# Kernel tuning notes

Hardware: AMD Instinct MI355X
Metric: run time of the kernel (lower is better)

Reference implementation:

```python
import jax, jax.numpy as jnp
import numpy as np

B, H, W, C = 16, 64, 64, 512
NH, HD = 16, 32
WH = WW = 8
SHIFT = 4
N = WH * WW
NWIN = (H // WH) * (W // WW)
EPS = 1e-6


def _rel_coords_table():
    rh = np.arange(-(WH - 1), WH, dtype=np.float32)
    rw = np.arange(-(WW - 1), WW, dtype=np.float32)
    t = np.expand_dims(np.transpose(np.stack(np.meshgrid(rh, rw)), (1, 2, 0)), 0)
    t[:, :, :, 0] /= WH - 1
    t[:, :, :, 1] /= WW - 1
    t *= 8
    t = np.sign(t) * np.log2(np.abs(t) + 1.0) / np.log2(8)
    return jnp.asarray(t, jnp.float32)  # (1, 2*WW-1, 2*WH-1, 2)


def _rel_pos_index():
    gx, gy = np.meshgrid(np.arange(WH), np.arange(WW))
    coords = np.stack([gy, gx]).reshape(2, -1)
    rel = (coords[:, :, None] - coords[:, None, :]).transpose(1, 2, 0)
    rel[:, :, 0] += WH - 1
    rel[:, :, 1] += WW - 1
    rel[:, :, 0] *= 2 * WW - 1
    return jnp.asarray(rel.sum(-1).reshape(-1), jnp.int32)  # (N*N,)


def _attn_mask():
    img = np.zeros((H, W), np.float32)
    cnt = 0
    for hs in (slice(0, -WH), slice(-WH, -SHIFT), slice(-SHIFT, None)):
        for ws in (slice(0, -WW), slice(-WW, -SHIFT), slice(-SHIFT, None)):
            img[hs, ws] = cnt
            cnt += 1
    mw = img.reshape(H // WH, WH, W // WW, WW).transpose(0, 2, 1, 3).reshape(-1, N)
    am = mw[:, None, :] - mw[:, :, None]
    return jnp.asarray(np.where(am == 0, 0.0, -100.0), jnp.float32)  # (nW, N, N)


REL_TABLE = _rel_coords_table()
REL_IDX = _rel_pos_index()
ATTN_MASK = _attn_mask()


def _ln(x, g, b):
    m = jnp.mean(x, -1, keepdims=True)
    v = jnp.var(x, -1, keepdims=True)
    return (x - m) * jax.lax.rsqrt(v + EPS) * g + b


def _forward(x, q_w, q_b, k_w, v_w, v_b, proj_w, proj_b, tau,
             cpb_w1, cpb_b1, cpb_w2, cpb_b2,
             norm1_g, norm1_b, norm2_g, norm2_b,
             mlp_w1, mlp_b1, mlp_w2, mlp_b2):
    shortcut = x
    xs = x.reshape(B, H, W, C)
    xs = jnp.roll(xs, shift=(-SHIFT, -SHIFT), axis=(1, 2))  # cyclic shift
    # window partition -> (B*nW, N, C)
    xw = xs.reshape(B, H // WH, WH, W // WW, WW, C).transpose(0, 1, 3, 2, 4, 5).reshape(-1, N, C)
    Bw = B * NWIN
    q = (xw @ q_w + q_b).reshape(Bw, N, NH, HD).transpose(0, 2, 1, 3)
    k = (xw @ k_w).reshape(Bw, N, NH, HD).transpose(0, 2, 1, 3)
    v = (xw @ v_w + v_b).reshape(Bw, N, NH, HD).transpose(0, 2, 1, 3)
    # cosine attention
    qn = jnp.linalg.norm(q, axis=-1)[..., :, None]
    kn = jnp.linalg.norm(k, axis=-1)[..., None, :]
    denom = jnp.maximum(qn * kn, 1e-6)
    attn = jnp.einsum('bhnd,bhmd->bhnm', q, k) / denom
    logit_scale = jnp.maximum(tau + jnp.log(10.0), 0.01)  # (1, NH, 1, 1)
    attn = attn * logit_scale
    # continuous relative position bias MLP
    tbl = jax.nn.relu(REL_TABLE @ cpb_w1 + cpb_b1) @ cpb_w2 + cpb_b2
    tbl = tbl.reshape(-1, NH)
    bias = tbl[REL_IDX].reshape(N, N, NH).transpose(2, 0, 1)
    bias = 16.0 * jax.nn.sigmoid(bias)
    attn = attn + bias[None]
    # shifted-window mask
    attn = attn.reshape(B, NWIN, NH, N, N) + ATTN_MASK[None, :, None]
    attn = jax.nn.softmax(attn.reshape(Bw, NH, N, N), axis=-1)
    out = jnp.einsum('bhnm,bhmd->bhnd', attn, v).transpose(0, 2, 1, 3).reshape(Bw, N, C)
    out = out @ proj_w + proj_b
    # window reverse + reverse shift
    out = out.reshape(B, H // WH, W // WW, WH, WW, C).transpose(0, 1, 3, 2, 4, 5).reshape(B, H, W, C)
    out = jnp.roll(out, shift=(SHIFT, SHIFT), axis=(1, 2)).reshape(B, H * W, C)
    # Swin-V2 post-norm residuals
    x = shortcut + _ln(out, norm1_g, norm1_b)
    h = jax.nn.gelu(x @ mlp_w1 + mlp_b1) @ mlp_w2 + mlp_b2
    x = x + _ln(h, norm2_g, norm2_b)
    return x


def setup_inputs() -> dict:
    key = jax.random.key(0)
    ks = jax.random.split(key, 10)
    s = 0.02
    return {
        'x': jax.random.normal(ks[0], (B, H * W, C), jnp.float32),
        'q_w': jax.random.normal(ks[1], (C, C), jnp.float32) * s,
        'q_b': jnp.zeros((C,), jnp.float32),
        'k_w': jax.random.normal(ks[2], (C, C), jnp.float32) * s,
        'v_w': jax.random.normal(ks[3], (C, C), jnp.float32) * s,
        'v_b': jnp.zeros((C,), jnp.float32),
        'proj_w': jax.random.normal(ks[4], (C, C), jnp.float32) * s,
        'proj_b': jnp.zeros((C,), jnp.float32),
        'tau': jax.random.normal(ks[5], (1, NH, 1, 1), jnp.float32) * s,
        'cpb_w1': jax.random.normal(ks[6], (2, 512), jnp.float32) * s,
        'cpb_b1': jnp.zeros((512,), jnp.float32),
        'cpb_w2': jax.random.normal(ks[7], (512, NH), jnp.float32) * s,
        'cpb_b2': jnp.zeros((NH,), jnp.float32),
        'norm1_g': jnp.ones((C,), jnp.float32),
        'norm1_b': jnp.zeros((C,), jnp.float32),
        'norm2_g': jnp.ones((C,), jnp.float32),
        'norm2_b': jnp.zeros((C,), jnp.float32),
        'mlp_w1': jax.random.normal(ks[8], (C, 4 * C), jnp.float32) * s,
        'mlp_b1': jnp.zeros((4 * C,), jnp.float32),
        'mlp_w2': jax.random.normal(ks[9], (4 * C, C), jnp.float32) * s,
        'mlp_b2': jnp.zeros((C,), jnp.float32),
    }


def reference(x, q_w, q_b, k_w, v_w, v_b, proj_w, proj_b, tau,
              cpb_w1, cpb_b1, cpb_w2, cpb_b2,
              norm1_g, norm1_b, norm2_g, norm2_b,
              mlp_w1, mlp_b1, mlp_w2, mlp_b2):
    return _forward(x, q_w, q_b, k_w, v_w, v_b, proj_w, proj_b, tau,
                    cpb_w1, cpb_b1, cpb_w2, cpb_b2,
                    norm1_g, norm1_b, norm2_g, norm2_b,
                    mlp_w1, mlp_b1, mlp_w2, mlp_b2)
```

## Files before the change

### kernel.cpp

```cpp
#include <hip/hip_runtime.h>
#include <cstdint>
#include <cstddef>

typedef __bf16 bf16x8 __attribute__((ext_vector_type(8)));
typedef float  f32x4  __attribute__((ext_vector_type(4)));
typedef unsigned short u16x8 __attribute__((ext_vector_type(8)));

__device__ __forceinline__ float bf2f(unsigned short u) {
  union { unsigned int u; float f; } v; v.u = ((unsigned int)u) << 16; return v.f;
}
__device__ __forceinline__ unsigned short f2bf(float f) {
  union { float f; unsigned int u; } v; v.f = f;
  return (unsigned short)((v.u + 0x7fffu + ((v.u >> 16) & 1u)) >> 16);
}
__device__ __forceinline__ bf16x8 as_bf(u16x8 u) {
  union { u16x8 a; bf16x8 b; } v; v.a = u; return v.b;
}
__device__ __forceinline__ void g2lds16(const void* g, void* l) {
  __builtin_amdgcn_global_load_lds((__attribute__((address_space(1))) void*)g,
                                   (__attribute__((address_space(3))) void*)l,
                                   16, 0, 0);
}

template<int EPI>
__global__ __launch_bounds__(512, 2) void gemm256(
    const unsigned short* __restrict__ A, const unsigned short* __restrict__ BT,
    const float* __restrict__ bias, unsigned short* __restrict__ C,
    int M, int N, int K)
{
  __shared__ __align__(16) unsigned short lds[2][2][2][128 * 64];
  const int tid = threadIdx.x;
  const int wave = tid >> 6, lane = tid & 63;
  const int lm = lane & 15, quad = lane >> 4;
  const int wm2 = wave >> 2, wn4 = wave & 3;
  const int ex = (lm & 7) << 3;

  const int nbx = (int)gridDim.x;
  const int nwg = nbx * (int)gridDim.y;
  const int flat = (int)blockIdx.y * nbx + (int)blockIdx.x;
  const int cpx = nwg >> 3;
  const int wg = (flat & 7) * cpx + (flat >> 3);
  const int bm = wg / nbx, bn = wg % nbx;

  const int NT = K >> 6;

  const int sl8 = lane >> 3;
  const int scol = ((lane & 7) ^ sl8) << 3;
  const int r0 = wave * 8 + sl8;
  const unsigned short* Abase = A + (size_t)(bm * 256 + r0) * K + scol;
  const unsigned short* Bbase = BT + (size_t)(bn * 256 + (r0 >> 5) * 64 + (r0 & 31)) * K + scol;

  auto stageA = [&](int bf, int sh, int koff) {
    const unsigned short* s = Abase + (size_t)(sh * 64) * K + koff;
    g2lds16(s,                   &lds[bf][0][sh][wave * 512]);
    g2lds16(s + (size_t)128 * K, &lds[bf][0][sh][4096 + wave * 512]);
  };
  auto stageB = [&](int bf, int sh, int koff) {
    const unsigned short* s = Bbase + (size_t)(sh * 32) * K + koff;
    g2lds16(s,                   &lds[bf][1][sh][wave * 512]);
    g2lds16(s + (size_t)128 * K, &lds[bf][1][sh][4096 + wave * 512]);
  };

  f32x4 acc[8][4];
#pragma unroll
  for (int i = 0; i < 8; i++)
#pragma unroll
    for (int j = 0; j < 4; j++) acc[i][j] = {0.f, 0.f, 0.f, 0.f};
  bf16x8 a[4][2], b0[2][2], b1[2][2];

  stageA(0, 0, 0); stageB(0, 0, 0); stageB(0, 1, 0); stageA(0, 1, 0);
  {
    const int k1 = (NT > 1 ? 64 : 0);
    stageA(1, 0, k1); stageB(1, 0, k1);
  }
  asm volatile("s_waitcnt vmcnt(4)" ::: "memory");
  __builtin_amdgcn_s_barrier();

  for (int t = 0; t < NT; ++t) {
    const int b = t & 1;
    const int kn1 = (t + 1 < NT ? t + 1 : NT - 1) << 6;
    const int kn2 = (t + 2 < NT ? t + 2 : NT - 1) << 6;

#pragma unroll
    for (int mi = 0; mi < 4; mi++)
#pragma unroll
      for (int ks = 0; ks < 2; ks++)
        a[mi][ks] = *(const bf16x8*)&lds[b][0][0][(wm2 * 64 + mi * 16 + lm) * 64 + ((ks * 32 + quad * 8) ^ ex)];
#pragma unroll
    for (int ni = 0; ni < 2; ni++)
#pragma unroll
      for (int ks = 0; ks < 2; ks++)
        b0[ni][ks] = *(const bf16x8*)&lds[b][1][0][(wn4 * 32 + ni * 16 + lm) * 64 + ((ks * 32 + quad * 8) ^ ex)];
    stageB(b ^ 1, 1, kn1);
    __builtin_amdgcn_s_barrier();
    __builtin_amdgcn_s_setprio(1);
#pragma unroll
    for (int mi = 0; mi < 4; mi++)
#pragma unroll
      for (int ni = 0; ni < 2; ni++)
#pragma unroll
        for (int ks = 0; ks < 2; ks++)
          acc[mi][ni] = __builtin_amdgcn_mfma_f32_16x16x32_bf16(a[mi][ks], b0[ni][ks], acc[mi][ni], 0, 0, 0);
    __builtin_amdgcn_s_setprio(0);
    asm volatile("s_waitcnt vmcnt(8)" ::: "memory");
    __builtin_amdgcn_s_barrier();

#pragma unroll
    for (int ni = 0; ni < 2; ni++)
#pragma unroll
      for (int ks = 0; ks < 2; ks++)
        b1[ni][ks] = *(const bf16x8*)&lds[b][1][1][(wn4 * 32 + ni * 16 + lm) * 64 + ((ks * 32 + quad * 8) ^ ex)];
    stageA(b ^ 1, 1, kn1);
    __builtin_amdgcn_s_barrier();
    __builtin_amdgcn_s_setprio(1);
#pragma unroll
    for (int mi = 0; mi < 4; mi++)
#pragma unroll
      for (int ni = 0; ni < 2; ni++)
#pragma unroll
        for (int ks = 0; ks < 2; ks++)
          acc[mi][2 + ni] = __builtin_amdgcn_mfma_f32_16x16x32_bf16(a[mi][ks], b1[ni][ks], acc[mi][2 + ni], 0, 0, 0);
    __builtin_amdgcn_s_setprio(0);
    asm volatile("s_waitcnt vmcnt(8)" ::: "memory");
    __builtin_amdgcn_s_barrier();

#pragma unroll
    for (int mi = 0; mi < 4; mi++)
#pragma unroll
      for (int ks = 0; ks < 2; ks++)
        a[mi][ks] = *(const bf16x8*)&lds[b][0][1][(wm2 * 64 + mi * 16 + lm) * 64 + ((ks * 32 + quad * 8) ^ ex)];
    stageA(b, 0, kn2);
    __builtin_amdgcn_s_barrier();
    __builtin_amdgcn_s_setprio(1);
#pragma unroll
    for (int mi = 0; mi < 4; mi++)
#pragma unroll
      for (int ni = 0; ni < 2; ni++)
#pragma unroll
        for (int ks = 0; ks < 2; ks++)
          acc[4 + mi][ni] = __builtin_amdgcn_mfma_f32_16x16x32_bf16(a[mi][ks], b0[ni][ks], acc[4 + mi][ni], 0, 0, 0);
    __builtin_amdgcn_s_setprio(0);
    asm volatile("s_waitcnt vmcnt(8)" ::: "memory");
    __builtin_amdgcn_s_barrier();

    stageB(b, 0, kn2);
    __builtin_amdgcn_s_barrier();
    __builtin_amdgcn_s_setprio(1);
#pragma unroll
    for (int mi = 0; mi < 4; mi++)
#pragma unroll
      for (int ni = 0; ni < 2; ni++)
#pragma unroll
        for (int ks = 0; ks < 2; ks++)
          acc[4 + mi][2 + ni] = __builtin_amdgcn_mfma_f32_16x16x32_bf16(a[mi][ks], b1[ni][ks], acc[4 + mi][2 + ni], 0, 0, 0);
    __builtin_amdgcn_s_setprio(0);
    asm volatile("s_waitcnt vmcnt(8)" ::: "memory");
    __builtin_amdgcn_s_barrier();
  }

  float bv[4];
#pragma unroll
  for (int jn = 0; jn < 4; jn++)
    bv[jn] = bias ? bias[bn * 256 + wn4 * 64 + jn * 16 + lm] : 0.f;
  const int rb = bm * 256 + wm2 * 128 + quad * 4;
  const int cb = bn * 256 + wn4 * 64 + lm;
#pragma unroll
  for (int im = 0; im < 8; im++)
#pragma unroll
    for (int jn = 0; jn < 4; jn++)
#pragma unroll
      for (int r = 0; r < 4; r++) {
        float v = acc[im][jn][r] + bv[jn];
        if (EPI == 1) {
          float xx = v;
          float u = 1.5957691216057308f * (xx + 0.044715f * xx * xx * xx);
          v = xx / (1.f + __expf(-u));
        }
        C[(size_t)(rb + im * 16 + r) * N + cb + jn * 16] = f2bf(v);
      }
}

__global__ __launch_bounds__(256) void transpose_cast(
    const float* __restrict__ W, unsigned short* __restrict__ WT, int K, int N)
{
  __shared__ float t[32][33];
  int bx = blockIdx.x, by = blockIdx.y;
  int tx = threadIdx.x & 31, ty = threadIdx.x >> 5;
#pragma unroll
  for (int j = 0; j < 4; j++)
    t[ty + j * 8][tx] = W[(size_t)(by * 32 + ty + j * 8) * N + bx * 32 + tx];
  __syncthreads();
#pragma unroll
  for (int j = 0; j < 4; j++)
    WT[(size_t)(bx * 32 + ty + j * 8) * K + by * 32 + tx] = f2bf(t[tx][ty + j * 8]);
}

__global__ __launch_bounds__(256) void shift_part(
    const float* __restrict__ x, unsigned short* __restrict__ xw)
{
  int t = blockIdx.x * 256 + threadIdx.x;
  int row = t >> 7;
  int c = (t & 127) * 4;
  int b = row >> 12, rw_ = row & 4095;
  int wi = rw_ >> 6, p = rw_ & 63;
  int hh = (((wi >> 3) * 8 + (p >> 3)) + 4) & 63;
  int ww = (((wi & 7) * 8 + (p & 7)) + 4) & 63;
  const float4 v = *(const float4*)&x[(((size_t)b * 4096) + hh * 64 + ww) * 512 + c];
  ushort4 o;
  o.x = f2bf(v.x); o.y = f2bf(v.y); o.z = f2bf(v.z); o.w = f2bf(v.w);
  *(ushort4*)&xw[(size_t)row * 512 + c] = o;
}

__global__ __launch_bounds__(256) void qkv_bias_kernel(
    const float* __restrict__ qb, const float* __restrict__ vb, float* __restrict__ o)
{
  int t = blockIdx.x * 256 + threadIdx.x;
  float v = 0.f;
  if (t < 512) v = qb[t];
  else if (t >= 1024) v = vb[t - 1024];
  o[t] = v;
}

__device__ __forceinline__ float relsc(int v) {
  float a = fabsf((float)v) * (8.0f / 7.0f);
  float r = log2f(a + 1.f) * (1.f / 3.f);
  return v < 0 ? -r : r;
}
__global__ __launch_bounds__(512) void cpb_kernel(
    const float* __restrict__ w1, const float* __restrict__ b1,
    const float* __restrict__ w2, const float* __restrict__ b2, float* __restrict__ tblT)
{
  __shared__ float hid[512];
  int p = blockIdx.x;
  int i = p / 15, j = p % 15;
  float fr = relsc(i - 7);
  float fc = relsc(j - 7);
  int t = threadIdx.x;
  float hv = fc * w1[t] + fr * w1[512 + t] + b1[t];
  hid[t] = fmaxf(hv, 0.f);
  __syncthreads();
  if (t < 16) {
    float s = b2[t];
    for (int u = 0; u < 512; u++) s += hid[u] * w2[u * 16 + t];
    tblT[t * 225 + p] = 16.f / (1.f + __expf(-s));
  }
}

__global__ __launch_bounds__(256) void attn_mfma(
    const unsigned short* __restrict__ QKV, const float* __restrict__ tau,
    const float* __restrict__ tblT, unsigned short* __restrict__ Om)
{
  __shared__ __align__(16) unsigned short Qs[64 * 32];
  __shared__ __align__(16) unsigned short Ks[64 * 32];
  __shared__ __align__(16) unsigned short Vs[64 * 32];
  __shared__ __align__(16) unsigned short VT[32 * 72];
  __shared__ __align__(16) unsigned short Pb[64 * 72];
  __shared__ float tblh[2][228];
  __shared__ int scode[64];

  const int tid = threadIdx.x;
  const int wave = tid >> 6, lane = tid & 63;
  const int lm = lane & 15, quad = lane >> 4;
  const int w = blockIdx.x >> 1;
  const int hbase = (blockIdx.x & 1) * 8;
  const int wi = w & 63, wr = wi >> 3, wc = wi & 7;
  const size_t wbase = (size_t)w * 64 * 1536;
  const size_t obase = (size_t)w * 64 * 512;

  if (tid < 64) {
    int p = tid;
    int rp = wr * 8 + (p >> 3), cp = wc * 8 + (p & 7);
    scode[p] = (rp < 56 ? 0 : (rp < 60 ? 1 : 2)) * 3 + (cp < 56 ? 0 : (cp < 60 ? 1 : 2));
  }

  const int srow = wave * 16 + (lane >> 2);
  const int scol = (lane & 3) * 8;
  unsigned short* qdst = &Qs[wave * 16 * 32];
  unsigned short* kdst = &Ks[wave * 16 * 32];
  unsigned short* vdst = &Vs[wave * 16 * 32];
  const size_t gs0 = wbase + (size_t)srow * 1536 + scol;

  {
    const size_t g = gs0 + (size_t)hbase * 32;
    g2lds16(QKV + g, qdst);
    g2lds16(QKV + g + 512, kdst);
    g2lds16(QKV + g + 1024, vdst);
    for (int e = tid; e < 225; e += 256) tblh[0][e] = tblT[hbase * 225 + e];
  }

  for (int hh = 0; hh < 8; hh++) {
    const int h = hbase + hh, cur = hh & 1;
    __syncthreads();

    u16x8 au = *(const u16x8*)&Qs[(wave * 16 + lm) * 32 + quad * 8];
    float qss = 0.f;
#pragma unroll
    for (int j = 0; j < 8; j++) { float f = bf2f(au[j]); qss += f * f; }
    qss += __shfl_xor(qss, 16, 64);
    qss += __shfl_xor(qss, 32, 64);
    const float qnv = sqrtf(qss);

    u16x8 bu[4]; float knv[4];
#pragma unroll
    for (int ni = 0; ni < 4; ni++) {
      bu[ni] = *(const u16x8*)&Ks[(ni * 16 + lm) * 32 + quad * 8];
      float kss = 0.f;
#pragma unroll
      for (int j = 0; j < 8; j++) { float f = bf2f(bu[ni][j]); kss += f * f; }
      kss += __shfl_xor(kss, 16, 64);
      kss += __shfl_xor(kss, 32, 64);
      knv[ni] = sqrtf(kss);
    }

    bf16x8 af = as_bf(au);
    f32x4 accS[4];
#pragma unroll
    for (int ni = 0; ni < 4; ni++) {
      f32x4 z = {0.f, 0.f, 0.f, 0.f};
      accS[ni] = __builtin_amdgcn_mfma_f32_16x16x32_bf16(af, as_bf(bu[ni]), z, 0, 0, 0);
    }

    for (int e = tid; e < 2048; e += 256) {
      int d = e & 31, q = e >> 5;
      VT[d * 72 + q] = Vs[q * 32 + d];
    }

    const float scale = fmaxf(tau[h] + 2.302585092994046f, 0.01f);
#pragma unroll
    for (int r = 0; r < 4; r++) {
      int p = wave * 16 + quad * 4 + r;
      float qnp = __shfl(qnv, quad * 4 + r, 64);
      int cp = scode[p];
      float sv[4];
#pragma unroll
      for (int ni = 0; ni < 4; ni++) {
        int q = ni * 16 + lm;
        float denom = fmaxf(qnp * knv[ni], 1e-6f);
        int dr = (p >> 3) - (q >> 3) + 7, dc = (p & 7) - (q & 7) + 7;
        float bv = tblh[cur][dr * 15 + dc];
        float mask = (cp == scode[q]) ? 0.f : -100.f;
        sv[ni] = accS[ni][r] * scale * __builtin_amdgcn_rcpf(denom) + bv + mask;
      }
      float m = fmaxf(fmaxf(sv[0], sv[1]), fmaxf(sv[2], sv[3]));
#pragma unroll
      for (int off = 1; off < 16; off <<= 1) m = fmaxf(m, __shfl_xor(m, off, 64));
      float s = 0.f;
#pragma unroll
      for (int ni = 0; ni < 4; ni++) { sv[ni] = __expf(sv[ni] - m); s += sv[ni]; }
#pragma unroll
      for (int off = 1; off < 16; off <<= 1) s += __shfl_xor(s, off, 64);
      float inv = __builtin_amdgcn_rcpf(s);
#pragma unroll
      for (int ni = 0; ni < 4; ni++)
        Pb[p * 72 + ni * 16 + lm] = f2bf(sv[ni] * inv);
    }

    __syncthreads();

    if (hh < 7) {
      const size_t g = gs0 + (size_t)(h + 1) * 32;
      g2lds16(QKV + g, qdst);
      g2lds16(QKV + g + 512, kdst);
      g2lds16(QKV + g + 1024, vdst);
      for (int e = tid; e < 225; e += 256) tblh[cur ^ 1][e] = tblT[(h + 1) * 225 + e];
    }

    bf16x8 paf[2];
#pragma unroll
    for (int kc = 0; kc < 2; kc++)
      paf[kc] = *reinterpret_cast<const bf16x8*>(&Pb[(wave * 16 + lm) * 72 + kc * 32 + quad * 8]);
    f32x4 accO[2];
#pragma unroll
    for (int n2 = 0; n2 < 2; n2++) {
      f32x4 z = {0.f, 0.f, 0.f, 0.f};
#pragma unroll
      for (int kc = 0; kc < 2; kc++) {
        bf16x8 vb = *reinterpret_cast<const bf16x8*>(&VT[(n2 * 16 + lm) * 72 + kc * 32 + quad * 8]);
        z = __builtin_amdgcn_mfma_f32_16x16x32_bf16(paf[kc], vb, z, 0, 0, 0);
      }
      accO[n2] = z;
    }
#pragma unroll
    for (int n2 = 0; n2 < 2; n2++)
#pragma unroll
      for (int r = 0; r < 4; r++) {
        int p = wave * 16 + quad * 4 + r;
        Om[obase + (size_t)p * 512 + h * 32 + n2 * 16 + lm] = f2bf(accO[n2][r]);
      }
  }
}

__global__ __launch_bounds__(256) void ln1_kernel(
    const float* __restrict__ x, const unsigned short* __restrict__ proj,
    const float* __restrict__ g, const float* __restrict__ b,
    unsigned short* __restrict__ x1b)
{
  __shared__ float r1[4], r2[4], stats[2];
  int tkn = blockIdx.x;
  int bb = tkn >> 12, s = tkn & 4095;
  int h_ = s >> 6, w_ = s & 63;
  int r = (h_ + 60) & 63, cc = (w_ + 60) & 63;
  int wi = (r >> 3) * 8 + (cc >> 3);
  int p = (r & 7) * 8 + (cc & 7);
  size_t src = ((size_t)bb * 4096 + wi * 64 + p) * 512;
  int c = threadIdx.x * 2;
  unsigned int pv = *(const unsigned int*)&proj[src + c];
  float v0 = bf2f((unsigned short)(pv & 0xffff)), v1 = bf2f((unsigned short)(pv >> 16));
  float ls = v0 + v1, lq = v0 * v0 + v1 * v1;
  for (int off = 32; off > 0; off >>= 1) {
    ls += __shfl_down(ls, off, 64);
    lq += __shfl_down(lq, off, 64);
  }
  int wv = threadIdx.x >> 6, ln = threadIdx.x & 63;
  if (ln == 0) { r1[wv] = ls; r2[wv] = lq; }
  __syncthreads();
  if (threadIdx.x == 0) {
    float S1 = r1[0] + r1[1] + r1[2] + r1[3];
    float S2 = r2[0] + r2[1] + r2[2] + r2[3];
    float mean = S1 * (1.f / 512.f);
    float var = S2 * (1.f / 512.f) - mean * mean;
    stats[0] = mean; stats[1] = rsqrtf(var + 1e-6f);
  }
  __syncthreads();
  float mean = stats[0], rstd = stats[1];
  size_t o = (size_t)tkn * 512 + c;
  float2 xv = *(const float2*)&x[o];
  float y0 = (v0 - mean) * rstd * g[c] + b[c] + xv.x;
  float y1 = (v1 - mean) * rstd * g[c + 1] + b[c + 1] + xv.y;
  unsigned int ov = (unsigned int)f2bf(y0) | ((unsigned int)f2bf(y1) << 16);
  *(unsigned int*)&x1b[o] = ov;
}

__global__ __launch_bounds__(256) void ln2_kernel(
    const unsigned short* __restrict__ x1b, const unsigned short* __restrict__ h2,
    const float* __restrict__ g, const float* __restrict__ b,
    float* __restrict__ out)
{
  __shared__ float r1[4], r2[4], stats[2];
  int tkn = blockIdx.x;
  int c = threadIdx.x * 2;
  size_t o = (size_t)tkn * 512 + c;
  unsigned int hv = *(const unsigned int*)&h2[o];
  float v0 = bf2f((unsigned short)(hv & 0xffff)), v1 = bf2f((unsigned short)(hv >> 16));
  float ls = v0 + v1, lq = v0 * v0 + v1 * v1;
  for (int off = 32; off > 0; off >>= 1) {
    ls += __shfl_down(ls, off, 64);
    lq += __shfl_down(lq, off, 64);
  }
  int wv = threadIdx.x >> 6, ln = threadIdx.x & 63;
  if (ln == 0) { r1[wv] = ls; r2[wv] = lq; }
  __syncthreads();
  if (threadIdx.x == 0) {
    float S1 = r1[0] + r1[1] + r1[2] + r1[3];
    float S2 = r2[0] + r2[1] + r2[2] + r2[3];
    float mean = S1 * (1.f / 512.f);
    float var = S2 * (1.f / 512.f) - mean * mean;
    stats[0] = mean; stats[1] = rsqrtf(var + 1e-6f);
  }
  __syncthreads();
  float mean = stats[0], rstd = stats[1];
  unsigned int xv = *(const unsigned int*)&x1b[o];
  float x0 = bf2f((unsigned short)(xv & 0xffff)), x1 = bf2f((unsigned short)(xv >> 16));
  float2 ov;
  ov.x = x0 + (v0 - mean) * rstd * g[c] + b[c];
  ov.y = x1 + (v1 - mean) * rstd * g[c + 1] + b[c + 1];
  *(float2*)&out[o] = ov;
}

extern "C" void kernel_launch(void* const* d_in, const int* in_sizes, int n_in,
                              void* d_out, int out_size, void* d_ws, size_t ws_size,
                              hipStream_t stream) {
  const float* x      = (const float*)d_in[0];
  const float* q_w    = (const float*)d_in[1];
  const float* q_b    = (const float*)d_in[2];
  const float* k_w    = (const float*)d_in[3];
  const float* v_w    = (const float*)d_in[4];
  const float* v_b    = (const float*)d_in[5];
  const float* proj_w = (const float*)d_in[6];
  const float* proj_b = (const float*)d_in[7];
  const float* tau    = (const float*)d_in[8];
  const float* cpb_w1 = (const float*)d_in[9];
  const float* cpb_b1 = (const float*)d_in[10];
  const float* cpb_w2 = (const float*)d_in[11];
  const float* cpb_b2 = (const float*)d_in[12];
  const float* n1g    = (const float*)d_in[13];
  const float* n1b    = (const float*)d_in[14];
  const float* n2g    = (const float*)d_in[15];
  const float* n2b    = (const float*)d_in[16];
  const float* mlp_w1 = (const float*)d_in[17];
  const float* mlp_b1 = (const float*)d_in[18];
  const float* mlp_w2 = (const float*)d_in[19];
  const float* mlp_b2 = (const float*)d_in[20];
  float* out = (float*)d_out;
  char* ws = (char*)d_ws;

  const size_t MB = 1048576;
  unsigned short* xw    = (unsigned short*)(ws + 0 * MB);
  unsigned short* Obuf  = (unsigned short*)(ws + 0 * MB);
  unsigned short* hbuf  = (unsigned short*)(ws + 0 * MB);
  unsigned short* qkv   = (unsigned short*)(ws + 64 * MB);
  unsigned short* projb = (unsigned short*)(ws + 64 * MB);
  unsigned short* x1b   = (unsigned short*)(ws + 128 * MB);
  unsigned short* h2b   = (unsigned short*)(ws + 192 * MB);
  unsigned short* qkvT = (unsigned short*)(ws + 320 * MB);
  unsigned short* pwT  = (unsigned short*)(ws + 320 * MB + 1572864);
  unsigned short* m1T  = (unsigned short*)(ws + 320 * MB + 2097152);
  unsigned short* m2T  = (unsigned short*)(ws + 320 * MB + 4194304);
  float* tbl           = (float*)         (ws + 320 * MB + 6291456);
  float* qkv_b         = (float*)         (ws + 320 * MB + 6307840);

  transpose_cast<<<dim3(16, 16), 256, 0, stream>>>(q_w,    qkvT,          512, 512);
  transpose_cast<<<dim3(16, 16), 256, 0, stream>>>(k_w,    qkvT + 262144, 512, 512);
  transpose_cast<<<dim3(16, 16), 256, 0, stream>>>(v_w,    qkvT + 524288, 512, 512);
  transpose_cast<<<dim3(16, 16), 256, 0, stream>>>(proj_w, pwT, 512, 512);
  transpose_cast<<<dim3(64, 16), 256, 0, stream>>>(mlp_w1, m1T, 512, 2048);
  transpose_cast<<<dim3(16, 64), 256, 0, stream>>>(mlp_w2, m2T, 2048, 512);
  qkv_bias_kernel<<<6, 256, 0, stream>>>(q_b, v_b, qkv_b);
  cpb_kernel<<<225, 512, 0, stream>>>(cpb_w1, cpb_b1, cpb_w2, cpb_b2, tbl);
  shift_part<<<32768, 256, 0, stream>>>(x, xw);
  gemm256<0><<<dim3(6, 256), 512, 0, stream>>>(xw, qkvT, qkv_b, qkv, 65536, 1536, 512);
  attn_mfma<<<2048, 256, 0, stream>>>(qkv, tau, tbl, Obuf);
  gemm256<0><<<dim3(2, 256), 512, 0, stream>>>(Obuf, pwT, proj_b, projb, 65536, 512, 512);
  ln1_kernel<<<65536, 256, 0, stream>>>(x, projb, n1g, n1b, x1b);
  for (int c2 = 0; c2 < 2; c2++) {
    const unsigned short* a = x1b + (size_t)c2 * 32768 * 512;
    unsigned short* h2p = h2b + (size_t)c2 * 32768 * 512;
    gemm256<1><<<dim3(8, 128), 512, 0, stream>>>(a, m1T, mlp_b1, hbuf, 32768, 2048, 512);
    gemm256<0><<<dim3(2, 128), 512, 0, stream>>>(hbuf, m2T, mlp_b2, h2p, 32768, 512, 2048);
  }
  ln2_kernel<<<65536, 256, 0, stream>>>(x1b, h2b, n2g, n2b, out);
}
```

Before: 1.005 ms.

## Make GEMM persistent with cross-tile prefetch; vectorize layernorms to one wave per token

The GEMM now launches a fixed 256 persistent workgroups, and each loops over several output tiles. During the last k-steps of the current tile it prefetches the next tile's first k-slices, which is meant to hide per-tile pipeline fill and launch overhead. Both layernorm kernels now use one wave per token with 8-element vector loads and a shuffle-only reduction, removing shared memory and block barriers. The risks are that 256 workgroups may under-fill the GPU's compute units, and that tile-count divisibility is assumed (T/256 must be an integer).

```diff
diff --git a/kernel.cpp b/kernel.cpp
--- a/kernel.cpp
+++ b/kernel.cpp
@@ -26,7 +26,7 @@
 __global__ __launch_bounds__(512, 2) void gemm256(
     const unsigned short* __restrict__ A, const unsigned short* __restrict__ BT,
     const float* __restrict__ bias, unsigned short* __restrict__ C,
-    int M, int N, int K)
+    int N, int K, int nbx, int T)
 {
   __shared__ __align__(16) unsigned short lds[2][2][2][128 * 64];
   const int tid = threadIdx.x;
@@ -35,149 +35,162 @@
   const int wm2 = wave >> 2, wn4 = wave & 3;
   const int ex = (lm & 7) << 3;
 
-  const int nbx = (int)gridDim.x;
-  const int nwg = nbx * (int)gridDim.y;
-  const int flat = (int)blockIdx.y * nbx + (int)blockIdx.x;
-  const int cpx = nwg >> 3;
-  const int wg = (flat & 7) * cpx + (flat >> 3);
-  const int bm = wg / nbx, bn = wg % nbx;
-
   const int NT = K >> 6;
+  const int cpx = T >> 3;
+  const int nit = T >> 8;
 
   const int sl8 = lane >> 3;
   const int scol = ((lane & 7) ^ sl8) << 3;
   const int r0 = wave * 8 + sl8;
-  const unsigned short* Abase = A + (size_t)(bm * 256 + r0) * K + scol;
-  const unsigned short* Bbase = BT + (size_t)(bn * 256 + (r0 >> 5) * 64 + (r0 & 31)) * K + scol;
-
-  auto stageA = [&](int bf, int sh, int koff) {
-    const unsigned short* s = Abase + (size_t)(sh * 64) * K + koff;
+  const int aro = r0;
+  const int bro = (r0 >> 5) * 64 + (r0 & 31);
+
+  auto stA = [&](const unsigned short* Ab, int bf, int sh, int koff) {
+    const unsigned short* s = Ab + (size_t)(sh * 64) * K + koff;
     g2lds16(s,                   &lds[bf][0][sh][wave * 512]);
     g2lds16(s + (size_t)128 * K, &lds[bf][0][sh][4096 + wave * 512]);
   };
-  auto stageB = [&](int bf, int sh, int koff) {
-    const unsigned short* s = Bbase + (size_t)(sh * 32) * K + koff;
+  auto stB = [&](const unsigned short* Bb, int bf, int sh, int koff) {
+    const unsigned short* s = Bb + (size_t)(sh * 32) * K + koff;
     g2lds16(s,                   &lds[bf][1][sh][wave * 512]);
     g2lds16(s + (size_t)128 * K, &lds[bf][1][sh][4096 + wave * 512]);
   };
 
+  int v = blockIdx.x;
+  int wg = (v & 7) * cpx + (v >> 3);
+  int bm = wg / nbx, bn = wg % nbx;
+  const unsigned short* curA = A + (size_t)(bm * 256 + aro) * K + scol;
+  const unsigned short* curB = BT + (size_t)(bn * 256 + bro) * K + scol;
+
   f32x4 acc[8][4];
-#pragma unroll
-  for (int i = 0; i < 8; i++)
-#pragma unroll
-    for (int j = 0; j < 4; j++) acc[i][j] = {0.f, 0.f, 0.f, 0.f};
   bf16x8 a[4][2], b0[2][2], b1[2][2];
 
-  stageA(0, 0, 0); stageB(0, 0, 0); stageB(0, 1, 0); stageA(0, 1, 0);
-  {
-    const int k1 = (NT > 1 ? 64 : 0);
-    stageA(1, 0, k1); stageB(1, 0, k1);
-  }
+  stA(curA, 0, 0, 0); stB(curB, 0, 0, 0); stB(curB, 0, 1, 0); stA(curA, 0, 1, 0);
+  stA(curA, 1, 0, 64); stB(curB, 1, 0, 64);
   asm volatile("s_waitcnt vmcnt(4)" ::: "memory");
   __builtin_amdgcn_s_barrier();
 
-  for (int t = 0; t < NT; ++t) {
-    const int b = t & 1;
-    const int kn1 = (t + 1 < NT ? t + 1 : NT - 1) << 6;
-    const int kn2 = (t + 2 < NT ? t + 2 : NT - 1) << 6;
-
-#pragma unroll
-    for (int mi = 0; mi < 4; mi++)
-#pragma unroll
-      for (int ks = 0; ks < 2; ks++)
-        a[mi][ks] = *(const bf16x8*)&lds[b][0][0][(wm2 * 64 + mi * 16 + lm) * 64 + ((ks * 32 + quad * 8) ^ ex)];
-#pragma unroll
-    for (int ni = 0; ni < 2; ni++)
-#pragma unroll
-      for (int ks = 0; ks < 2; ks++)
-        b0[ni][ks] = *(const bf16x8*)&lds[b][1][0][(wn4 * 32 + ni * 16 + lm) * 64 + ((ks * 32 + quad * 8) ^ ex)];
-    stageB(b ^ 1, 1, kn1);
-    __builtin_amdgcn_s_barrier();
-    __builtin_amdgcn_s_setprio(1);
-#pragma unroll
-    for (int mi = 0; mi < 4; mi++)
+  for (int it = 0; it < nit; ++it) {
+    int vN = v + 256;
+    int wgN = (it + 1 < nit) ? ((vN & 7) * cpx + (vN >> 3)) : wg;
+    int bmN = wgN / nbx, bnN = wgN % nbx;
+    const unsigned short* nxtA = A + (size_t)(bmN * 256 + aro) * K + scol;
+    const unsigned short* nxtB = BT + (size_t)(bnN * 256 + bro) * K + scol;
+
+#pragma unroll
+    for (int i = 0; i < 8; i++)
+#pragma unroll
+      for (int j = 0; j < 4; j++) acc[i][j] = {0.f, 0.f, 0.f, 0.f};
+
+    for (int t = 0; t < NT; ++t) {
+      const int b = t & 1;
+      const unsigned short *A1, *B1, *A2, *B2; int k1, k2;
+      if (t + 1 < NT) { A1 = curA; B1 = curB; k1 = (t + 1) << 6; }
+      else            { A1 = nxtA; B1 = nxtB; k1 = 0; }
+      if (t + 2 < NT) { A2 = curA; B2 = curB; k2 = (t + 2) << 6; }
+      else            { A2 = nxtA; B2 = nxtB; k2 = (t + 2 - NT) << 6; }
+
+#pragma unroll
+      for (int mi = 0; mi < 4; mi++)
+#pragma unroll
+        for (int ks = 0; ks < 2; ks++)
+          a[mi][ks] = *(const bf16x8*)&lds[b][0][0][(wm2 * 64 + mi * 16 + lm) * 64 + ((ks * 32 + quad * 8) ^ ex)];
 #pragma unroll
       for (int ni = 0; ni < 2; ni++)
 #pragma unroll
         for (int ks = 0; ks < 2; ks++)
-          acc[mi][ni] = __builtin_amdgcn_mfma_f32_16x16x32_bf16(a[mi][ks], b0[ni][ks], acc[mi][ni], 0, 0, 0);
-    __builtin_amdgcn_s_setprio(0);
-    asm volatile("s_waitcnt vmcnt(8)" ::: "memory");
-    __builtin_amdgcn_s_barrier();
-
-#pragma unroll
-    for (int ni = 0; ni < 2; ni++)
-#pragma unroll
-      for (int ks = 0; ks < 2; ks++)
-        b1[ni][ks] = *(const bf16x8*)&lds[b][1][1][(wn4 * 32 + ni * 16 + lm) * 64 + ((ks * 32 + quad * 8) ^ ex)];
-    stageA(b ^ 1, 1, kn1);
-    __builtin_amdgcn_s_barrier();
-    __builtin_amdgcn_s_setprio(1);
-#pragma unroll
-    for (int mi = 0; mi < 4; mi++)
+          b0[ni][ks] = *(const bf16x8*)&lds[b][1][0][(wn4 * 32 + ni * 16 + lm) * 64 + ((ks * 32 + quad * 8) ^ ex)];
+      stB(B1, b ^ 1, 1, k1);
+      __builtin_amdgcn_s_barrier();
+      __builtin_amdgcn_s_setprio(1);
+#pragma unroll
+      for (int mi = 0; mi < 4; mi++)
+#pragma unroll
+        for (int ni = 0; ni < 2; ni++)
+#pragma unroll
+          for (int ks = 0; ks < 2; ks++)
+            acc[mi][ni] = __builtin_amdgcn_mfma_f32_16x16x32_bf16(a[mi][ks], b0[ni][ks], acc[mi][ni], 0, 0, 0);
+      __builtin_amdgcn_s_setprio(0);
+      asm volatile("s_waitcnt vmcnt(8)" ::: "memory");
+      __builtin_amdgcn_s_barrier();
+
 #pragma unroll
       for (int ni = 0; ni < 2; ni++)
 #pragma unroll
         for (int ks = 0; ks < 2; ks++)
-          acc[mi][2 + ni] = __builtin_amdgcn_mfma_f32_16x16x32_bf16(a[mi][ks], b1[ni][ks], acc[mi][2 + ni], 0, 0, 0);
-    __builtin_amdgcn_s_setprio(0);
-    asm volatile("s_waitcnt vmcnt(8)" ::: "memory");
-    __builtin_amdgcn_s_barrier();
-
-#pragma unroll
-    for (int mi = 0; mi < 4; mi++)
-#pragma unroll
-      for (int ks = 0; ks < 2; ks++)
-        a[mi][ks] = *(const bf16x8*)&lds[b][0][1][(wm2 * 64 + mi * 16 + lm) * 64 + ((ks * 32 + quad * 8) ^ ex)];
-    stageA(b, 0, kn2);
-    __builtin_amdgcn_s_barrier();
-    __builtin_amdgcn_s_setprio(1);
-#pragma unroll
-    for (int mi = 0; mi < 4; mi++)
-#pragma unroll
-      for (int ni = 0; ni < 2; ni++)
+          b1[ni][ks] = *(const bf16x8*)&lds[b][1][1][(wn4 * 32 + ni * 16 + lm) * 64 + ((ks * 32 + quad * 8) ^ ex)];
+      stA(A1, b ^ 1, 1, k1);
+      __builtin_amdgcn_s_barrier();
+      __builtin_amdgcn_s_setprio(1);
+#pragma unroll
+      for (int mi = 0; mi < 4; mi++)
+#pragma unroll
+        for (int ni = 0; ni < 2; ni++)
+#pragma unroll
+          for (int ks = 0; ks < 2; ks++)
+            acc[mi][2 + ni] = __builtin_amdgcn_mfma_f32_16x16x32_bf16(a[mi][ks], b1[ni][ks], acc[mi][2 + ni], 0, 0, 0);
+      __builtin_amdgcn_s_setprio(0);
+      asm volatile("s_waitcnt vmcnt(8)" ::: "memory");
+      __builtin_amdgcn_s_barrier();
+
+#pragma unroll
+      for (int mi = 0; mi < 4; mi++)
 #pragma unroll
         for (int ks = 0; ks < 2; ks++)
-          acc[4 + mi][ni] = __builtin_amdgcn_mfma_f32_16x16x32_bf16(a[mi][ks], b0[ni][ks], acc[4 + mi][ni], 0, 0, 0);
-    __builtin_amdgcn_s_setprio(0);
-    asm volatile("s_waitcnt vmcnt(8)" ::: "memory");
-    __builtin_amdgcn_s_barrier();
-
-    stageB(b, 0, kn2);
-    __builtin_amdgcn_s_barrier();
-    __builtin_amdgcn_s_setprio(1);
-#pragma unroll
-    for (int mi = 0; mi < 4; mi++)
-#pragma unroll
-      for (int ni = 0; ni < 2; ni++)
-#pragma unroll
-        for (int ks = 0; ks < 2; ks++)
-          acc[4 + mi][2 + ni] = __builtin_amdgcn_mfma_f32_16x16x32_bf16(a[mi][ks], b1[ni][ks], acc[4 + mi][2 + ni], 0, 0, 0);
-    __builtin_amdgcn_s_setprio(0);
-    asm volatile("s_waitcnt vmcnt(8)" ::: "memory");
-    __builtin_amdgcn_s_barrier();
-  }
-
-  float bv[4];
-#pragma unroll
-  for (int jn = 0; jn < 4; jn++)
-    bv[jn] = bias ? bias[bn * 256 + wn4 * 64 + jn * 16 + lm] : 0.f;
-  const int rb = bm * 256 + wm2 * 128 + quad * 4;
-  const int cb = bn * 256 + wn4 * 64 + lm;
-#pragma unroll
-  for (int im = 0; im < 8; im++)
+          a[mi][ks] = *(const bf16x8*)&lds[b][0][1][(wm2 * 64 + mi * 16 + lm) * 64 + ((ks * 32 + quad * 8) ^ ex)];
+      stA(A2, b, 0, k2);
+      __builtin_amdgcn_s_barrier();
+      __builtin_amdgcn_s_setprio(1);
+#pragma unroll
+      for (int mi = 0; mi < 4; mi++)
+#pragma unroll
+        for (int ni = 0; ni < 2; ni++)
+#pragma unroll
+          for (int ks = 0; ks < 2; ks++)
+            acc[4 + mi][ni] = __builtin_amdgcn_mfma_f32_16x16x32_bf16(a[mi][ks], b0[ni][ks], acc[4 + mi][ni], 0, 0, 0);
+      __builtin_amdgcn_s_setprio(0);
+      asm volatile("s_waitcnt vmcnt(8)" ::: "memory");
+      __builtin_amdgcn_s_barrier();
+
+      stB(B2, b, 0, k2);
+      __builtin_amdgcn_s_barrier();
+      __builtin_amdgcn_s_setprio(1);
+#pragma unroll
+      for (int mi = 0; mi < 4; mi++)
+#pragma unroll
+        for (int ni = 0; ni < 2; ni++)
+#pragma unroll
+          for (int ks = 0; ks < 2; ks++)
+            acc[4 + mi][2 + ni] = __builtin_amdgcn_mfma_f32_16x16x32_bf16(a[mi][ks], b1[ni][ks], acc[4 + mi][2 + ni], 0, 0, 0);
+      __builtin_amdgcn_s_setprio(0);
+      asm volatile("s_waitcnt vmcnt(8)" ::: "memory");
+      __builtin_amdgcn_s_barrier();
+    }
+
+    float bv[4];
 #pragma unroll
     for (int jn = 0; jn < 4; jn++)
-#pragma unroll
-      for (int r = 0; r < 4; r++) {
-        float v = acc[im][jn][r] + bv[jn];
-        if (EPI == 1) {
-          float xx = v;
-          float u = 1.5957691216057308f * (xx + 0.044715f * xx * xx * xx);
-          v = xx / (1.f + __expf(-u));
+      bv[jn] = bias ? bias[bn * 256 + wn4 * 64 + jn * 16 + lm] : 0.f;
+    const int rb = bm * 256 + wm2 * 128 + quad * 4;
+    const int cb = bn * 256 + wn4 * 64 + lm;
+#pragma unroll
+    for (int im = 0; im < 8; im++)
+#pragma unroll
+      for (int jn = 0; jn < 4; jn++)
+#pragma unroll
+        for (int r = 0; r < 4; r++) {
+          float vvv = acc[im][jn][r] + bv[jn];
+          if (EPI == 1) {
+            float xx = vvv;
+            float u = 1.5957691216057308f * (xx + 0.044715f * xx * xx * xx);
+            vvv = xx / (1.f + __expf(-u));
+          }
+          C[(size_t)(rb + im * 16 + r) * N + cb + jn * 16] = f2bf(vvv);
         }
-        C[(size_t)(rb + im * 16 + r) * N + cb + jn * 16] = f2bf(v);
-      }
+
+    v = vN; wg = wgN; bm = bmN; bn = bnN; curA = nxtA; curB = nxtB;
+  }
+  asm volatile("s_waitcnt vmcnt(0)" ::: "memory");
 }
 
 __global__ __launch_bounds__(256) void transpose_cast(
@@ -395,40 +408,40 @@
     const float* __restrict__ g, const float* __restrict__ b,
     unsigned short* __restrict__ x1b)
 {
-  __shared__ float r1[4], r2[4], stats[2];
-  int tkn = blockIdx.x;
+  int tkn = blockIdx.x * 4 + (threadIdx.x >> 6);
+  int lane = threadIdx.x & 63;
   int bb = tkn >> 12, s = tkn & 4095;
   int h_ = s >> 6, w_ = s & 63;
   int r = (h_ + 60) & 63, cc = (w_ + 60) & 63;
   int wi = (r >> 3) * 8 + (cc >> 3);
   int p = (r & 7) * 8 + (cc & 7);
-  size_t src = ((size_t)bb * 4096 + wi * 64 + p) * 512;
-  int c = threadIdx.x * 2;
-  unsigned int pv = *(const unsigned int*)&proj[src + c];
-  float v0 = bf2f((unsigned short)(pv & 0xffff)), v1 = bf2f((unsigned short)(pv >> 16));
-  float ls = v0 + v1, lq = v0 * v0 + v1 * v1;
-  for (int off = 32; off > 0; off >>= 1) {
-    ls += __shfl_down(ls, off, 64);
-    lq += __shfl_down(lq, off, 64);
-  }
-  int wv = threadIdx.x >> 6, ln = threadIdx.x & 63;
-  if (ln == 0) { r1[wv] = ls; r2[wv] = lq; }
-  __syncthreads();
-  if (threadIdx.x == 0) {
-    float S1 = r1[0] + r1[1] + r1[2] + r1[3];
-    float S2 = r2[0] + r2[1] + r2[2] + r2[3];
-    float mean = S1 * (1.f / 512.f);
-    float var = S2 * (1.f / 512.f) - mean * mean;
-    stats[0] = mean; stats[1] = rsqrtf(var + 1e-6f);
-  }
-  __syncthreads();
-  float mean = stats[0], rstd = stats[1];
+  size_t src = ((size_t)bb * 4096 + wi * 64 + p) * 512 + lane * 8;
+  u16x8 pv = *(const u16x8*)&proj[src];
+  float v[8]; float ls = 0.f, lq = 0.f;
+#pragma unroll
+  for (int j = 0; j < 8; j++) { v[j] = bf2f(pv[j]); ls += v[j]; lq += v[j] * v[j]; }
+#pragma unroll
+  for (int off = 1; off < 64; off <<= 1) {
+    ls += __shfl_xor(ls, off, 64);
+    lq += __shfl_xor(lq, off, 64);
+  }
+  float mean = ls * (1.f / 512.f);
+  float rstd = rsqrtf(lq * (1.f / 512.f) - mean * mean + 1e-6f);
+  int c = lane * 8;
   size_t o = (size_t)tkn * 512 + c;
-  float2 xv = *(const float2*)&x[o];
-  float y0 = (v0 - mean) * rstd * g[c] + b[c] + xv.x;
-  float y1 = (v1 - mean) * rstd * g[c + 1] + b[c + 1] + xv.y;
-  unsigned int ov = (unsigned int)f2bf(y0) | ((unsigned int)f2bf(y1) << 16);
-  *(unsigned int*)&x1b[o] = ov;
+  float4 xa = *(const float4*)&x[o], xb = *(const float4*)&x[o + 4];
+  float4 ga = *(const float4*)&g[c], gb = *(const float4*)&g[c + 4];
+  float4 ba = *(const float4*)&b[c], bb4 = *(const float4*)&b[c + 4];
+  u16x8 ov;
+  ov[0] = f2bf((v[0] - mean) * rstd * ga.x + ba.x + xa.x);
+  ov[1] = f2bf((v[1] - mean) * rstd * ga.y + ba.y + xa.y);
+  ov[2] = f2bf((v[2] - mean) * rstd * ga.z + ba.z + xa.z);
+  ov[3] = f2bf((v[3] - mean) * rstd * ga.w + ba.w + xa.w);
+  ov[4] = f2bf((v[4] - mean) * rstd * gb.x + bb4.x + xb.x);
+  ov[5] = f2bf((v[5] - mean) * rstd * gb.y + bb4.y + xb.y);
+  ov[6] = f2bf((v[6] - mean) * rstd * gb.z + bb4.z + xb.z);
+  ov[7] = f2bf((v[7] - mean) * rstd * gb.w + bb4.w + xb.w);
+  *(u16x8*)&x1b[o] = ov;
 }
 
 __global__ __launch_bounds__(256) void ln2_kernel(
@@ -436,35 +449,35 @@
     const float* __restrict__ g, const float* __restrict__ b,
     float* __restrict__ out)
 {
-  __shared__ float r1[4], r2[4], stats[2];
-  int tkn = blockIdx.x;
-  int c = threadIdx.x * 2;
+  int tkn = blockIdx.x * 4 + (threadIdx.x >> 6);
+  int lane = threadIdx.x & 63;
+  int c = lane * 8;
   size_t o = (size_t)tkn * 512 + c;
-  unsigned int hv = *(const unsigned int*)&h2[o];
-  float v0 = bf2f((unsigned short)(hv & 0xffff)), v1 = bf2f((unsigned short)(hv >> 16));
-  float ls = v0 + v1, lq = v0 * v0 + v1 * v1;
-  for (int off = 32; off > 0; off >>= 1) {
-    ls += __shfl_down(ls, off, 64);
-    lq += __shfl_down(lq, off, 64);
-  }
-  int wv = threadIdx.x >> 6, ln = threadIdx.x & 63;
-  if (ln == 0) { r1[wv] = ls; r2[wv] = lq; }
-  __syncthreads();
-  if (threadIdx.x == 0) {
-    float S1 = r1[0] + r1[1] + r1[2] + r1[3];
-    float S2 = r2[0] + r2[1] + r2[2] + r2[3];
-    float mean = S1 * (1.f / 512.f);
-    float var = S2 * (1.f / 512.f) - mean * mean;
-    stats[0] = mean; stats[1] = rsqrtf(var + 1e-6f);
-  }
-  __syncthreads();
-  float mean = stats[0], rstd = stats[1];
-  unsigned int xv = *(const unsigned int*)&x1b[o];
-  float x0 = bf2f((unsigned short)(xv & 0xffff)), x1 = bf2f((unsigned short)(xv >> 16));
-  float2 ov;
-  ov.x = x0 + (v0 - mean) * rstd * g[c] + b[c];
-  ov.y = x1 + (v1 - mean) * rstd * g[c + 1] + b[c + 1];
-  *(float2*)&out[o] = ov;
+  u16x8 hv = *(const u16x8*)&h2[o];
+  float v[8]; float ls = 0.f, lq = 0.f;
+#pragma unroll
+  for (int j = 0; j < 8; j++) { v[j] = bf2f(hv[j]); ls += v[j]; lq += v[j] * v[j]; }
+#pragma unroll
+  for (int off = 1; off < 64; off <<= 1) {
+    ls += __shfl_xor(ls, off, 64);
+    lq += __shfl_xor(lq, off, 64);
+  }
+  float mean = ls * (1.f / 512.f);
+  float rstd = rsqrtf(lq * (1.f / 512.f) - mean * mean + 1e-6f);
+  u16x8 xv = *(const u16x8*)&x1b[o];
+  float4 ga = *(const float4*)&g[c], gb = *(const float4*)&g[c + 4];
+  float4 ba = *(const float4*)&b[c], bb4 = *(const float4*)&b[c + 4];
+  float4 oa, ob;
+  oa.x = bf2f(xv[0]) + (v[0] - mean) * rstd * ga.x + ba.x;
+  oa.y = bf2f(xv[1]) + (v[1] - mean) * rstd * ga.y + ba.y;
+  oa.z = bf2f(xv[2]) + (v[2] - mean) * rstd * ga.z + ba.z;
+  oa.w = bf2f(xv[3]) + (v[3] - mean) * rstd * ga.w + ba.w;
+  ob.x = bf2f(xv[4]) + (v[4] - mean) * rstd * gb.x + bb4.x;
+  ob.y = bf2f(xv[5]) + (v[5] - mean) * rstd * gb.y + bb4.y;
+  ob.z = bf2f(xv[6]) + (v[6] - mean) * rstd * gb.z + bb4.z;
+  ob.w = bf2f(xv[7]) + (v[7] - mean) * rstd * gb.w + bb4.w;
+  *(float4*)&out[o] = oa;
+  *(float4*)&out[o + 4] = ob;
 }
 
 extern "C" void kernel_launch(void* const* d_in, const int* in_sizes, int n_in,
@@ -518,15 +531,15 @@
   qkv_bias_kernel<<<6, 256, 0, stream>>>(q_b, v_b, qkv_b);
   cpb_kernel<<<225, 512, 0, stream>>>(cpb_w1, cpb_b1, cpb_w2, cpb_b2, tbl);
   shift_part<<<32768, 256, 0, stream>>>(x, xw);
-  gemm256<0><<<dim3(6, 256), 512, 0, stream>>>(xw, qkvT, qkv_b, qkv, 65536, 1536, 512);
+  gemm256<0><<<256, 512, 0, stream>>>(xw, qkvT, qkv_b, qkv, 1536, 512, 6, 1536);
   attn_mfma<<<2048, 256, 0, stream>>>(qkv, tau, tbl, Obuf);
-  gemm256<0><<<dim3(2, 256), 512, 0, stream>>>(Obuf, pwT, proj_b, projb, 65536, 512, 512);
-  ln1_kernel<<<65536, 256, 0, stream>>>(x, projb, n1g, n1b, x1b);
+  gemm256<0><<<256, 512, 0, stream>>>(Obuf, pwT, proj_b, projb, 512, 512, 2, 512);
+  ln1_kernel<<<16384, 256, 0, stream>>>(x, projb, n1g, n1b, x1b);
   for (int c2 = 0; c2 < 2; c2++) {
     const unsigned short* a = x1b + (size_t)c2 * 32768 * 512;
     unsigned short* h2p = h2b + (size_t)c2 * 32768 * 512;
-    gemm256<1><<<dim3(8, 128), 512, 0, stream>>>(a, m1T, mlp_b1, hbuf, 32768, 2048, 512);
-    gemm256<0><<<dim3(2, 128), 512, 0, stream>>>(hbuf, m2T, mlp_b2, h2p, 32768, 512, 2048);
-  }
-  ln2_kernel<<<65536, 256, 0, stream>>>(x1b, h2b, n2g, n2b, out);
-}
+    gemm256<1><<<256, 512, 0, stream>>>(a, m1T, mlp_b1, hbuf, 2048, 512, 8, 1024);
+    gemm256<0><<<256, 512, 0, stream>>>(hbuf, m2T, mlp_b2, h2p, 512, 2048, 2, 256);
+  }
+  ln2_kernel<<<16384, 256, 0, stream>>>(x1b, h2b, n2g, n2b, out);
+}
```

Result: faster. 925.8 us (-7.8%).
